# Optimization experiments

Measured on AMD Instinct MI355X. Metric: run time of the kernel, lower is better.

## Reference

```python
import jax, jax.numpy as jnp
import numpy as np

NUM_HEADS = 8
HEAD_SIZE = 64  # hidden_dim // num_heads = 512 // 8
SCALE = 1.0 / np.sqrt(HEAD_SIZE).astype(np.float32)
CAUSAL = True


def setup_inputs() -> dict:
    key = jax.random.key(0)
    k1, k2, k3 = jax.random.split(key, 3)
    b, s, d = 4, 2048, 512
    x = jax.random.normal(k1, (b, s, d), dtype=jnp.float32)
    w_qkv = jax.random.normal(k2, (d, 3 * d), dtype=jnp.float32) * 0.02
    b_qkv = jnp.zeros((3 * d,), dtype=jnp.float32)
    w_out = jax.random.normal(k3, (d, d), dtype=jnp.float32) * 0.02
    b_out = jnp.zeros((d,), dtype=jnp.float32)
    return {"x": x, "w_qkv": w_qkv, "b_qkv": b_qkv, "w_out": w_out, "b_out": b_out}


def reference(x, w_qkv, b_qkv, w_out, b_out):
    b, s, d = x.shape
    h, hd = NUM_HEADS, HEAD_SIZE
    qkv = x @ w_qkv + b_qkv                      # (b, s, 3d)
    q, k, v = jnp.split(qkv, 3, axis=-1)
    # (b, s, d) -> (b, h, s, hd)
    q = q.reshape(b, s, h, hd).transpose(0, 2, 1, 3)
    k = k.reshape(b, s, h, hd).transpose(0, 2, 1, 3)
    v = v.reshape(b, s, h, hd).transpose(0, 2, 1, 3)
    scores = jnp.einsum('bhqd,bhkd->bhqk', q, k) * SCALE  # (b, h, s, s)
    if CAUSAL:
        causal_mask = jnp.triu(jnp.ones((s, s), dtype=bool), k=1)
        scores = jnp.where(causal_mask, -jnp.inf, scores)
    attn = jax.nn.softmax(scores, axis=-1)
    out = jnp.einsum('bhqk,bhkd->bhqd', attn, v)          # (b, h, s, hd)
    out = out.transpose(0, 2, 1, 3).reshape(b, s, d)
    return out @ w_out + b_out
```

## Files before the change

kernel.cpp:

```cpp
#include <hip/hip_runtime.h>
#include <hip/hip_bf16.h>

#define BATCH 4
#define SEQ   2048
#define DM    512
#define NH    8
#define HD    64
#define PART  (BATCH*NH*SEQ*HD)
#define QSCALE 0.18033688f

typedef unsigned short u16;
typedef unsigned int   u32;
typedef __bf16 bf16x8 __attribute__((ext_vector_type(8)));
typedef float  f32x4  __attribute__((ext_vector_type(4)));

__device__ __forceinline__ u16 f2bf(float f) {
    union { float f; u32 u; } v; v.f = f;
    u32 r = v.u + 0x7fffu + ((v.u >> 16) & 1u);
    return (u16)(r >> 16);
}

__device__ __forceinline__ void glds16(const u16* g, u16* lds) {
    __builtin_amdgcn_global_load_lds(
        (const __attribute__((address_space(1))) void*)g,
        (__attribute__((address_space(3))) void*)lds, 16, 0, 0);
}

__global__ __launch_bounds__(256) void prep_k(
    const float* __restrict__ x, u16* __restrict__ xb,
    const float* __restrict__ w_qkv, u16* __restrict__ t_qkv,
    const float* __restrict__ w_out, u16* __restrict__ t_out)
{
    __shared__ u16 Ts[64][72];
    const int z = blockIdx.z, bx = blockIdx.x, t = threadIdx.x;

    if (z == 0) {
        const int n8 = PART / 8;
        for (int i = bx * 256 + t; i < n8; i += 512 * 256) {
            float4 a = *(const float4*)(x + (size_t)i * 8);
            float4 b = *(const float4*)(x + (size_t)i * 8 + 4);
            union { uint4 v; u16 s[8]; } o;
            o.s[0] = f2bf(a.x); o.s[1] = f2bf(a.y);
            o.s[2] = f2bf(a.z); o.s[3] = f2bf(a.w);
            o.s[4] = f2bf(b.x); o.s[5] = f2bf(b.y);
            o.s[6] = f2bf(b.z); o.s[7] = f2bf(b.w);
            *(uint4*)(xb + (size_t)i * 8) = o.v;
        }
        return;
    }
    const int N = (z == 1) ? 3 * DM : DM;
    const int ntiles = N / 64;
    if (bx >= ntiles * 8) return;
    const float* W = (z == 1) ? w_qkv : w_out;
    u16* Wt = (z == 1) ? t_qkv : t_out;
    const int n0 = (bx % ntiles) * 64, k0 = (bx / ntiles) * 64;

    #pragma unroll
    for (int l = 0; l < 4; ++l) {
        int idx = l * 1024 + t * 4;
        int r = idx >> 6, c = idx & 63;
        float4 v = *(const float4*)(W + (size_t)(k0 + r) * N + n0 + c);
        Ts[c + 0][r] = f2bf(v.x);
        Ts[c + 1][r] = f2bf(v.y);
        Ts[c + 2][r] = f2bf(v.z);
        Ts[c + 3][r] = f2bf(v.w);
    }
    __syncthreads();
    #pragma unroll
    for (int l = 0; l < 2; ++l) {
        int idx = l * 256 + t;
        int row = idx >> 3, ch = idx & 7;
        *(uint4*)(Wt + (size_t)(n0 + row) * DM + k0 + ch * 8) =
            *(const uint4*)(&Ts[row][ch * 8]);
    }
}

template<int MODE>
__global__ __launch_bounds__(256) void gemm_k(
    const u16* __restrict__ A, const u16* __restrict__ Bt,
    const float* __restrict__ bias, void* __restrict__ outv,
    int M, int N, int K)
{
    constexpr int BM = (MODE == 1) ? 64 : 128;
    constexpr int NI = (MODE == 1) ? 2 : 4;

    __shared__ __align__(16) u16 As[2][BM * 32];
    __shared__ __align__(16) u16 Bs[2][128 * 32];

    const int tid  = threadIdx.x;
    const int bm0  = blockIdx.x * BM;
    const int bn0  = blockIdx.y * 128;
    const int wave = tid >> 6, lane = tid & 63;
    const int l16  = lane & 15, quad = lane >> 4;
    const int wr   = (MODE == 1) ? 0 : (wave & 1) * 64;
    const int wc   = (MODE == 1) ? wave * 32 : (wave >> 1) * 64;

    const int srow = (lane >> 2);
    const int scol = (lane & 3) * 8;
    const int arow = (MODE == 1) ? (wave * 16) : (wave * 32);
    const u16* Ag = A + (size_t)(bm0 + arow + srow) * K + scol;
    const u16* Bg = Bt + (size_t)(bn0 + wave * 32 + srow) * K + scol;
    const int wofsA = arow * 32;
    const int wofsB = (wave * 32) * 32;

    f32x4 acc[4][NI];
    #pragma unroll
    for (int i = 0; i < 4; ++i)
        #pragma unroll
        for (int j = 0; j < NI; ++j)
            acc[i][j] = (f32x4){0.f, 0.f, 0.f, 0.f};

    glds16(Ag, &As[0][wofsA]);
    if (MODE == 0) glds16(Ag + (size_t)16 * K, &As[0][wofsA + 16 * 32]);
    glds16(Bg,                  &Bs[0][wofsB]);
    glds16(Bg + (size_t)16 * K, &Bs[0][wofsB + 16 * 32]);
    __syncthreads();

    const int NIT = K >> 5;
    for (int it = 0; it < NIT; ++it) {
        const int cur = it & 1;
        if (it + 1 < NIT) {
            const int nx = cur ^ 1;
            const int k0 = (it + 1) << 5;
            glds16(Ag + k0, &As[nx][wofsA]);
            if (MODE == 0) glds16(Ag + k0 + (size_t)16 * K, &As[nx][wofsA + 16 * 32]);
            glds16(Bg + k0,                  &Bs[nx][wofsB]);
            glds16(Bg + k0 + (size_t)16 * K, &Bs[nx][wofsB + 16 * 32]);
        }

        bf16x8 af[4], bfr[NI];
        #pragma unroll
        for (int mi = 0; mi < 4; ++mi)
            af[mi] = *(const bf16x8*)(&As[cur][(wr + mi * 16 + l16) * 32 + quad * 8]);
        #pragma unroll
        for (int ni = 0; ni < NI; ++ni)
            bfr[ni] = *(const bf16x8*)(&Bs[cur][(wc + ni * 16 + l16) * 32 + quad * 8]);
        #pragma unroll
        for (int mi = 0; mi < 4; ++mi)
            #pragma unroll
            for (int ni = 0; ni < NI; ++ni)
                acc[mi][ni] = __builtin_amdgcn_mfma_f32_16x16x32_bf16(
                    af[mi], bfr[ni], acc[mi][ni], 0, 0, 0);
        __syncthreads();
    }

    #pragma unroll
    for (int mi = 0; mi < 4; ++mi) {
        #pragma unroll
        for (int ni = 0; ni < NI; ++ni) {
            int col = bn0 + wc + ni * 16 + l16;
            float bv = bias[col];
            int row0 = bm0 + wr + mi * 16 + quad * 4;
            float v[4];
            #pragma unroll
            for (int reg = 0; reg < 4; ++reg) v[reg] = acc[mi][ni][reg] + bv;

            if (MODE == 1) {
                #pragma unroll
                for (int reg = 0; reg < 4; ++reg)
                    ((float*)outv)[(size_t)(row0 + reg) * N + col] = v[reg];
            } else {
                u16* ws = (u16*)outv;
                int part = col >> 9, wi = col & 511;
                int h = wi >> 6, e = wi & 63;
                int b = row0 >> 11, s0 = row0 & 2047;
                if (part == 2) {
                    union { u16 q[4]; uint2 u; } pk;
                    #pragma unroll
                    for (int reg = 0; reg < 4; ++reg) pk.q[reg] = f2bf(v[reg]);
                    *(uint2*)(ws + (size_t)2 * PART +
                              ((size_t)(b * NH + h) * HD + e) * SEQ + s0) = pk.u;
                } else {
                    float scl = (part == 0) ? QSCALE : 1.0f;
                    #pragma unroll
                    for (int reg = 0; reg < 4; ++reg)
                        ws[(size_t)part * PART +
                           ((size_t)(b * NH + h) * SEQ + s0 + reg) * HD + e] =
                            f2bf(v[reg] * scl);
                }
            }
        }
    }
}

__global__ __launch_bounds__(256) void attn_k(
    const u16* __restrict__ Q, const u16* __restrict__ K,
    const u16* __restrict__ Vt, u16* __restrict__ O)
{
    __shared__ __align__(16) u16 KsB[2][64 * 64];
    __shared__ __align__(16) u16 VtB[2][64 * 64];
    __shared__ __align__(16) u16 Ps[64][72];

    const int bh = blockIdx.x;
    const int pair = blockIdx.y;
    const int tid = threadIdx.x, wave = tid >> 6, lane = tid & 63;
    const int l16 = lane & 15, quad = lane >> 4;
    const size_t baseK = (size_t)bh * SEQ * HD;
    const size_t baseV = (size_t)bh * HD * SEQ;
    const int b = bh >> 3, h = bh & 7;
    const int row64 = wave * 16 + quad * 4;

    const int sub = lane >> 3;
    const int lcx = (lane & 7) ^ sub;
    const u16* kg = K  + baseK + (size_t)((wave * 16 + sub) * 64)   + lcx * 8;
    const u16* vg = Vt + baseV + (size_t)((wave * 16 + sub) * 2048) + lcx * 8;
    u16* ksd = &KsB[0][wave * 1024];
    u16* vtd = &VtB[0][wave * 1024];

    #pragma unroll
    for (int phase = 0; phase < 2; ++phase) {
        const int qt = phase ? pair : (31 - pair);
        const size_t baseQ = baseK + (size_t)qt * 64 * HD;

        #pragma unroll
        for (int r = 0; r < 2; ++r) {
            int chunk = r * 256 + tid;
            int row = chunk >> 3, c8 = (chunk & 7) << 3;
            *(uint4*)(&Ps[row][c8]) = *(const uint4*)(Q + baseQ + row * 64 + c8);
        }
        __syncthreads();
        bf16x8 qf[2];
        #pragma unroll
        for (int d0 = 0; d0 < 2; ++d0)
            qf[d0] = *(const bf16x8*)(&Ps[wave * 16 + l16][d0 * 32 + quad * 8]);
        __syncthreads();

        glds16(kg,            ksd);
        glds16(kg + 8 * 64,   ksd + 512);
        glds16(vg,            vtd);
        glds16(vg + 8 * 2048, vtd + 512);
        __syncthreads();

        float l_part[4] = {0.f, 0.f, 0.f, 0.f};
        f32x4 o_acc[4];
        #pragma unroll
        for (int i = 0; i < 4; ++i) o_acc[i] = (f32x4){0.f, 0.f, 0.f, 0.f};

        for (int kt = 0; kt <= qt; ++kt) {
            const int cur = kt & 1;
            if (kt < qt) {
                const int nx = (cur ^ 1) * 4096;
                glds16(kg + (size_t)(kt + 1) * 4096,          ksd + nx);
                glds16(kg + (size_t)(kt + 1) * 4096 + 8 * 64, ksd + nx + 512);
                glds16(vg + (size_t)(kt + 1) * 64,            vtd + nx);
                glds16(vg + (size_t)(kt + 1) * 64 + 8 * 2048, vtd + nx + 512);
            }

            bf16x8 kf[2][4], vf[2][4];
            #pragma unroll
            for (int d0 = 0; d0 < 2; ++d0)
                #pragma unroll
                for (int nt = 0; nt < 4; ++nt) {
                    int pc = (d0 * 4 + quad) ^ (l16 & 7);
                    kf[d0][nt] = *(const bf16x8*)
                        (&KsB[cur][(nt * 16 + l16) * 64 + pc * 8]);
                    vf[d0][nt] = *(const bf16x8*)
                        (&VtB[cur][(nt * 16 + l16) * 64 + pc * 8]);
                }

            f32x4 s[4];
            #pragma unroll
            for (int nt = 0; nt < 4; ++nt) s[nt] = (f32x4){0.f, 0.f, 0.f, 0.f};
            #pragma unroll
            for (int d0 = 0; d0 < 2; ++d0)
                #pragma unroll
                for (int nt = 0; nt < 4; ++nt)
                    s[nt] = __builtin_amdgcn_mfma_f32_16x16x32_bf16(
                        qf[d0], kf[d0][nt], s[nt], 0, 0, 0);

            const bool diag = (kt == qt);
            #pragma unroll
            for (int nt = 0; nt < 4; ++nt) {
                int cl = nt * 16 + l16;
                float p[4];
                #pragma unroll
                for (int reg = 0; reg < 4; ++reg) {
                    p[reg] = __builtin_amdgcn_exp2f(s[nt][reg]);
                    if (diag && cl > row64 + reg) p[reg] = 0.f;
                    l_part[reg] += p[reg];
                }
                union { __hip_bfloat162 hh; u16 s2[2]; } pk01, pk23;
                pk01.hh = __float22bfloat162_rn(float2{p[0], p[1]});
                pk23.hh = __float22bfloat162_rn(float2{p[2], p[3]});
                Ps[row64 + 0][cl] = pk01.s2[0];
                Ps[row64 + 1][cl] = pk01.s2[1];
                Ps[row64 + 2][cl] = pk23.s2[0];
                Ps[row64 + 3][cl] = pk23.s2[1];
            }

            #pragma unroll
            for (int k0 = 0; k0 < 2; ++k0) {
                bf16x8 ap = *(const bf16x8*)
                    (&Ps[wave * 16 + l16][k0 * 32 + quad * 8]);
                #pragma unroll
                for (int dt = 0; dt < 4; ++dt)
                    o_acc[dt] = __builtin_amdgcn_mfma_f32_16x16x32_bf16(
                        ap, vf[k0][dt], o_acc[dt], 0, 0, 0);
            }
            __syncthreads();
        }

        float l_i[4];
        #pragma unroll
        for (int reg = 0; reg < 4; ++reg) {
            float l = l_part[reg];
            #pragma unroll
            for (int off = 1; off < 16; off <<= 1)
                l += __shfl_xor(l, off);
            l_i[reg] = l;
        }
        #pragma unroll
        for (int dt = 0; dt < 4; ++dt) {
            #pragma unroll
            for (int reg = 0; reg < 4; ++reg) {
                int srow = qt * 64 + row64 + reg;
                float v = o_acc[dt][reg] / l_i[reg];
                size_t idx = (((size_t)(b * SEQ + srow)) * NH + h) * HD
                             + dt * 16 + l16;
                O[idx] = f2bf(v);
            }
        }
    }
}

extern "C" void kernel_launch(void* const* d_in, const int* in_sizes, int n_in,
                              void* d_out, int out_size, void* d_ws, size_t ws_size,
                              hipStream_t stream) {
    const float* x     = (const float*)d_in[0];
    const float* w_qkv = (const float*)d_in[1];
    const float* b_qkv = (const float*)d_in[2];
    const float* w_out = (const float*)d_in[3];
    const float* b_out = (const float*)d_in[4];

    u16* qkv    = (u16*)d_ws;
    u16* attn   = qkv + (size_t)3 * PART;
    u16* xb     = attn + (size_t)PART;
    u16* wt_qkv = xb + (size_t)PART;
    u16* wt_out = wt_qkv + (size_t)(3 * DM) * DM;

    const int M = BATCH * SEQ;

    prep_k<<<dim3(512, 1, 3), 256, 0, stream>>>(x, xb, w_qkv, wt_qkv,
                                                w_out, wt_out);

    dim3 g1(M / 128, (3 * DM) / 128);
    gemm_k<0><<<g1, 256, 0, stream>>>(xb, wt_qkv, b_qkv, qkv, M, 3 * DM, DM);

    dim3 g2(BATCH * NH, 16);
    attn_k<<<g2, 256, 0, stream>>>(qkv, qkv + PART, qkv + 2 * (size_t)PART, attn);

    dim3 g3(M / 64, DM / 128);
    gemm_k<1><<<g3, 256, 0, stream>>>(attn, wt_out, b_out, (float*)d_out, M, DM, DM);
}
```

Measured before the change: 151.1 us.

## Software-pipeline PV with delayed softmax tiles and stage QKV epilogue through LDS

```diff
diff --git a/kernel.cpp b/kernel.cpp
--- a/kernel.cpp
+++ b/kernel.cpp
@@ -86,6 +86,7 @@
 
     __shared__ __align__(16) u16 As[2][BM * 32];
     __shared__ __align__(16) u16 Bs[2][128 * 32];
+    __shared__ __align__(16) u16 epi[128 * 72];
 
     const int tid  = threadIdx.x;
     const int bm0  = blockIdx.x * BM;
@@ -144,41 +145,73 @@
         __syncthreads();
     }
 
-    #pragma unroll
-    for (int mi = 0; mi < 4; ++mi) {
-        #pragma unroll
-        for (int ni = 0; ni < NI; ++ni) {
-            int col = bn0 + wc + ni * 16 + l16;
-            float bv = bias[col];
-            int row0 = bm0 + wr + mi * 16 + quad * 4;
-            float v[4];
-            #pragma unroll
-            for (int reg = 0; reg < 4; ++reg) v[reg] = acc[mi][ni][reg] + bv;
-
-            if (MODE == 1) {
+    if (MODE == 1) {
+        #pragma unroll
+        for (int mi = 0; mi < 4; ++mi)
+            #pragma unroll
+            for (int ni = 0; ni < NI; ++ni) {
+                int col = bn0 + wc + ni * 16 + l16;
+                float bv = bias[col];
+                int row0 = bm0 + wr + mi * 16 + quad * 4;
                 #pragma unroll
                 for (int reg = 0; reg < 4; ++reg)
-                    ((float*)outv)[(size_t)(row0 + reg) * N + col] = v[reg];
+                    ((float*)outv)[(size_t)(row0 + reg) * N + col] =
+                        acc[mi][ni][reg] + bv;
+            }
+    } else {
+        u16* ws = (u16*)outv;
+        const int part = bn0 >> 9;
+        const int h0   = (bn0 & 511) >> 6;
+        const int bq   = bm0 >> 11, s0 = bm0 & 2047;
+
+        #pragma unroll
+        for (int hh = 0; hh < 2; ++hh) {
+            if ((wave >> 1) == hh) {
+                #pragma unroll
+                for (int mi = 0; mi < 4; ++mi)
+                    #pragma unroll
+                    for (int ni = 0; ni < 4; ++ni) {
+                        int ce  = ni * 16 + l16;
+                        float bv = bias[bn0 + wc + ce - 0];
+                        int row0 = wr + mi * 16 + quad * 4;
+                        if (part < 2) {
+                            float scl = (part == 0) ? QSCALE : 1.0f;
+                            #pragma unroll
+                            for (int reg = 0; reg < 4; ++reg)
+                                epi[(row0 + reg) * 72 + ce] =
+                                    f2bf((acc[mi][ni][reg] + bv) * scl);
+                        } else {
+                            union { u16 q[4]; uint2 u; } pk;
+                            #pragma unroll
+                            for (int reg = 0; reg < 4; ++reg)
+                                pk.q[reg] = f2bf(acc[mi][ni][reg] + bv);
+                            *(uint2*)(&epi[ce * 144 + row0]) = pk.u;
+                        }
+                    }
+            }
+            __syncthreads();
+            if (part < 2) {
+                #pragma unroll
+                for (int l = 0; l < 4; ++l) {
+                    int idx = l * 256 + tid;
+                    int r = idx >> 3, e8 = (idx & 7) * 8;
+                    uint4 v = *(const uint4*)(&epi[r * 72 + e8]);
+                    *(uint4*)(ws + (size_t)part * PART +
+                              (((size_t)(bq * NH + h0 + hh) * SEQ) + s0 + r) * HD
+                              + e8) = v;
+                }
             } else {
-                u16* ws = (u16*)outv;
-                int part = col >> 9, wi = col & 511;
-                int h = wi >> 6, e = wi & 63;
-                int b = row0 >> 11, s0 = row0 & 2047;
-                if (part == 2) {
-                    union { u16 q[4]; uint2 u; } pk;
-                    #pragma unroll
-                    for (int reg = 0; reg < 4; ++reg) pk.q[reg] = f2bf(v[reg]);
-                    *(uint2*)(ws + (size_t)2 * PART +
-                              ((size_t)(b * NH + h) * HD + e) * SEQ + s0) = pk.u;
-                } else {
-                    float scl = (part == 0) ? QSCALE : 1.0f;
-                    #pragma unroll
-                    for (int reg = 0; reg < 4; ++reg)
-                        ws[(size_t)part * PART +
-                           ((size_t)(b * NH + h) * SEQ + s0 + reg) * HD + e] =
-                            f2bf(v[reg] * scl);
-                }
-            }
+                #pragma unroll
+                for (int l = 0; l < 4; ++l) {
+                    int idx = l * 256 + tid;
+                    int e = idx >> 4, sc = (idx & 15) * 8;
+                    uint4 v = *(const uint4*)(&epi[e * 144 + sc]);
+                    *(uint4*)(ws + (size_t)2 * PART +
+                              (((size_t)(bq * NH + h0 + hh) * HD) + e) * SEQ
+                              + s0 + sc) = v;
+                }
+            }
+            __syncthreads();
         }
     }
 }
@@ -188,8 +221,8 @@
     const u16* __restrict__ Vt, u16* __restrict__ O)
 {
     __shared__ __align__(16) u16 KsB[2][64 * 64];
-    __shared__ __align__(16) u16 VtB[2][64 * 64];
-    __shared__ __align__(16) u16 Ps[64][72];
+    __shared__ __align__(16) u16 VtB[3][64 * 64];
+    __shared__ __align__(16) u16 Ps[2][64][72];
 
     const int bh = blockIdx.x;
     const int pair = blockIdx.y;
@@ -212,18 +245,20 @@
         const int qt = phase ? pair : (31 - pair);
         const size_t baseQ = baseK + (size_t)qt * 64 * HD;
 
+        __syncthreads();
+
         #pragma unroll
         for (int r = 0; r < 2; ++r) {
             int chunk = r * 256 + tid;
             int row = chunk >> 3, c8 = (chunk & 7) << 3;
-            *(uint4*)(&Ps[row][c8]) = *(const uint4*)(Q + baseQ + row * 64 + c8);
+            *(uint4*)(&Ps[0][row][c8]) =
+                *(const uint4*)(Q + baseQ + row * 64 + c8);
         }
         __syncthreads();
         bf16x8 qf[2];
         #pragma unroll
         for (int d0 = 0; d0 < 2; ++d0)
-            qf[d0] = *(const bf16x8*)(&Ps[wave * 16 + l16][d0 * 32 + quad * 8]);
-        __syncthreads();
+            qf[d0] = *(const bf16x8*)(&Ps[0][wave * 16 + l16][d0 * 32 + quad * 8]);
 
         glds16(kg,            ksd);
         glds16(kg + 8 * 64,   ksd + 512);
@@ -237,27 +272,24 @@
         for (int i = 0; i < 4; ++i) o_acc[i] = (f32x4){0.f, 0.f, 0.f, 0.f};
 
         for (int kt = 0; kt <= qt; ++kt) {
-            const int cur = kt & 1;
             if (kt < qt) {
-                const int nx = (cur ^ 1) * 4096;
-                glds16(kg + (size_t)(kt + 1) * 4096,          ksd + nx);
-                glds16(kg + (size_t)(kt + 1) * 4096 + 8 * 64, ksd + nx + 512);
-                glds16(vg + (size_t)(kt + 1) * 64,            vtd + nx);
-                glds16(vg + (size_t)(kt + 1) * 64 + 8 * 2048, vtd + nx + 512);
-            }
-
-            bf16x8 kf[2][4], vf[2][4];
+                const int kx = ((kt + 1) & 1) * 4096;
+                const int vx = ((kt + 1) % 3) * 4096;
+                glds16(kg + (size_t)(kt + 1) * 4096,          ksd + kx);
+                glds16(kg + (size_t)(kt + 1) * 4096 + 8 * 64, ksd + kx + 512);
+                glds16(vg + (size_t)(kt + 1) * 64,            vtd + vx);
+                glds16(vg + (size_t)(kt + 1) * 64 + 8 * 2048, vtd + vx + 512);
+            }
+
+            bf16x8 kf[2][4];
             #pragma unroll
             for (int d0 = 0; d0 < 2; ++d0)
                 #pragma unroll
                 for (int nt = 0; nt < 4; ++nt) {
                     int pc = (d0 * 4 + quad) ^ (l16 & 7);
                     kf[d0][nt] = *(const bf16x8*)
-                        (&KsB[cur][(nt * 16 + l16) * 64 + pc * 8]);
-                    vf[d0][nt] = *(const bf16x8*)
-                        (&VtB[cur][(nt * 16 + l16) * 64 + pc * 8]);
-                }
-
+                        (&KsB[kt & 1][(nt * 16 + l16) * 64 + pc * 8]);
+                }
             f32x4 s[4];
             #pragma unroll
             for (int nt = 0; nt < 4; ++nt) s[nt] = (f32x4){0.f, 0.f, 0.f, 0.f};
@@ -267,6 +299,28 @@
                 for (int nt = 0; nt < 4; ++nt)
                     s[nt] = __builtin_amdgcn_mfma_f32_16x16x32_bf16(
                         qf[d0], kf[d0][nt], s[nt], 0, 0, 0);
+
+            if (kt > 0) {
+                const int pb = (kt - 1) & 1, vb = (kt - 1) % 3;
+                bf16x8 vf[2][4];
+                #pragma unroll
+                for (int k0 = 0; k0 < 2; ++k0)
+                    #pragma unroll
+                    for (int dt = 0; dt < 4; ++dt) {
+                        int pc = (k0 * 4 + quad) ^ (l16 & 7);
+                        vf[k0][dt] = *(const bf16x8*)
+                            (&VtB[vb][(dt * 16 + l16) * 64 + pc * 8]);
+                    }
+                #pragma unroll
+                for (int k0 = 0; k0 < 2; ++k0) {
+                    bf16x8 ap = *(const bf16x8*)
+                        (&Ps[pb][wave * 16 + l16][k0 * 32 + quad * 8]);
+                    #pragma unroll
+                    for (int dt = 0; dt < 4; ++dt)
+                        o_acc[dt] = __builtin_amdgcn_mfma_f32_16x16x32_bf16(
+                            ap, vf[k0][dt], o_acc[dt], 0, 0, 0);
+                }
+            }
 
             const bool diag = (kt == qt);
             #pragma unroll
@@ -279,25 +333,37 @@
                     if (diag && cl > row64 + reg) p[reg] = 0.f;
                     l_part[reg] += p[reg];
                 }
-                union { __hip_bfloat162 hh; u16 s2[2]; } pk01, pk23;
-                pk01.hh = __float22bfloat162_rn(float2{p[0], p[1]});
-                pk23.hh = __float22bfloat162_rn(float2{p[2], p[3]});
-                Ps[row64 + 0][cl] = pk01.s2[0];
-                Ps[row64 + 1][cl] = pk01.s2[1];
-                Ps[row64 + 2][cl] = pk23.s2[0];
-                Ps[row64 + 3][cl] = pk23.s2[1];
-            }
-
+                union { __hip_bfloat162 hh2; u16 s2[2]; } pk01, pk23;
+                pk01.hh2 = __float22bfloat162_rn(float2{p[0], p[1]});
+                pk23.hh2 = __float22bfloat162_rn(float2{p[2], p[3]});
+                Ps[kt & 1][row64 + 0][cl] = pk01.s2[0];
+                Ps[kt & 1][row64 + 1][cl] = pk01.s2[1];
+                Ps[kt & 1][row64 + 2][cl] = pk23.s2[0];
+                Ps[kt & 1][row64 + 3][cl] = pk23.s2[1];
+            }
+            __syncthreads();
+        }
+
+        {
+            const int pb = qt & 1, vb = qt % 3;
+            bf16x8 vf[2][4];
+            #pragma unroll
+            for (int k0 = 0; k0 < 2; ++k0)
+                #pragma unroll
+                for (int dt = 0; dt < 4; ++dt) {
+                    int pc = (k0 * 4 + quad) ^ (l16 & 7);
+                    vf[k0][dt] = *(const bf16x8*)
+                        (&VtB[vb][(dt * 16 + l16) * 64 + pc * 8]);
+                }
             #pragma unroll
             for (int k0 = 0; k0 < 2; ++k0) {
                 bf16x8 ap = *(const bf16x8*)
-                    (&Ps[wave * 16 + l16][k0 * 32 + quad * 8]);
+                    (&Ps[pb][wave * 16 + l16][k0 * 32 + quad * 8]);
                 #pragma unroll
                 for (int dt = 0; dt < 4; ++dt)
                     o_acc[dt] = __builtin_amdgcn_mfma_f32_16x16x32_bf16(
                         ap, vf[k0][dt], o_acc[dt], 0, 0, 0);
             }
-            __syncthreads();
         }
 
         float l_i[4];
```

After: 155.1 us. 2.6% more time.
